# Kernel optimization log

Hardware: AMD Instinct MI355X
Metric: run time of the kernel (lower is better)

The kernel has to match this reference:

```python
import jax, jax.numpy as jnp
import numpy as np

E = 16        # num_experts
H = 1024      # hidden_size
I = 768       # moe_intermediate_size
TOP_K = 2     # num_experts_per_tok
B, S = 1, 2048


def setup_inputs() -> dict:
    key = jax.random.key(0)
    ks = jax.random.split(key, 5)
    scale = 0.02
    return {
        "hidden_states": jax.random.normal(ks[0], (B, S, H), dtype=jnp.float32),
        "gate_w": jax.random.normal(ks[1], (E, H), dtype=jnp.float32) * scale,
        "gate_proj": jax.random.normal(ks[2], (E, I, H), dtype=jnp.float32) * scale,
        "up_proj": jax.random.normal(ks[3], (E, I, H), dtype=jnp.float32) * scale,
        "down_proj": jax.random.normal(ks[4], (E, H, I), dtype=jnp.float32) * scale,
    }


def reference(hidden_states, gate_w, gate_proj, up_proj, down_proj):
    b, s, h = hidden_states.shape
    x = hidden_states.reshape(-1, h)                        # [T, H]
    T = x.shape[0]

    # Router: logits -> fp32 softmax -> top-k -> renormalize (norm_topk_prob=True)
    router_logits = x @ gate_w.T                            # [T, E]
    probs = jax.nn.softmax(router_logits.astype(jnp.float32), axis=-1)
    top_vals, top_idx = jax.lax.top_k(probs, TOP_K)         # [T, k]
    top_vals = top_vals / jnp.sum(top_vals, axis=-1, keepdims=True)

    # Dense combine-weight matrix [T, E] (zero for unrouted experts)
    rw = jnp.zeros((T, E), dtype=jnp.float32)
    rw = rw.at[jnp.arange(T)[:, None], top_idx].add(top_vals)
    rw = rw.astype(hidden_states.dtype)

    # Expert SwiGLU MLPs (dense-over-experts reference for the grouped GEMM)
    g = jnp.einsum("th,eih->eti", x, gate_proj)             # [E, T, I]
    u = jnp.einsum("th,eih->eti", x, up_proj)               # [E, T, I]
    hmid = jax.nn.silu(g) * u                                # [E, T, I]
    expert_out = jnp.einsum("eti,ehi->eth", hmid, down_proj)  # [E, T, H]

    # Weighted combine
    out = jnp.einsum("eth,te->th", expert_out, rw)          # [T, H]
    return out.reshape(b, s, h)
```

## Files before the change

kernel.cpp:

```cpp
#include <hip/hip_runtime.h>
#include <hip/hip_bf16.h>
#include <cmath>

constexpr int T = 2048;
constexpr int H = 1024;
constexpr int I = 768;
constexpr int E = 16;
constexpr int WMAX = 48;

constexpr int CVT_ITEMS = 768 * 3;
constexpr int RTR_BLOCKS = T / 8;
constexpr int CS = 2056;

typedef short short8  __attribute__((ext_vector_type(8)));
typedef short short4v __attribute__((ext_vector_type(4)));
typedef float f32x4   __attribute__((ext_vector_type(4)));

__device__ __forceinline__ short f2bf(float f) {
    __hip_bfloat16 h = __float2bfloat16(f);
    return *reinterpret_cast<short*>(&h);
}

__device__ __forceinline__ short8 pack8(float4 a, float4 b) {
    short8 v = {f2bf(a.x), f2bf(a.y), f2bf(a.z), f2bf(a.w),
                f2bf(b.x), f2bf(b.y), f2bf(b.z), f2bf(b.w)};
    return v;
}

__device__ __forceinline__ int sw(int r, int kg) {
    return r * 32 + (((kg + (r >> 1)) & 3) << 3);
}

__device__ __forceinline__ bool find_item(const int* __restrict__ cnt, int bx,
                                          int& e_o, int& t0_o, int& n_o) {
    int c = 0;
    #pragma unroll
    for (int e = 0; e < E; ++e) {
        int n = cnt[e];
        int m = (n + 127) >> 7;
        if (bx < c + m) { e_o = e; t0_o = (bx - c) << 7; n_o = n; return true; }
        c += m;
    }
    return false;
}

__global__ __launch_bounds__(256) void prep_kernel(
    const float* __restrict__ x,
    const float* __restrict__ gw,
    const float* __restrict__ gp,
    const float* __restrict__ up,
    const float* __restrict__ dp,
    short* __restrict__ xb,
    short* __restrict__ wtg,
    short* __restrict__ wtu,
    short* __restrict__ wtd,
    int* __restrict__ cnt,
    int* __restrict__ entries,
    float* __restrict__ wlist)
{
    __shared__ short lds[8 * CS];
    __shared__ float lg[8][16][2];

    const int tid = threadIdx.x;
    const int bid = blockIdx.x;

    if (bid < CVT_ITEMS) {
        const float* src; short* dst; int K;
        if (bid < 1536) {
            const int mat = bid >= 768;
            const int id3 = mat ? bid - 768 : bid;
            const int e = id3 / 48, rem = id3 - e * 48;
            const int rb = rem >> 2, kq = rem & 3;
            K = H;
            src = (mat ? up : gp) + (size_t)e * I * H + (size_t)(rb * 64) * H + kq * 256;
            dst = (mat ? wtu : wtg) + ((size_t)(e * 12 + rb) * 32 + kq * 8) * 2048;
        } else {
            const int id3 = bid - 1536;
            const int e = id3 / 48, rem = id3 - e * 48;
            const int rb = rem / 3, kq = rem - rb * 3;
            K = I;
            src = dp + (size_t)e * H * I + (size_t)(rb * 64) * I + kq * 256;
            dst = wtd + ((size_t)(e * 16 + rb) * 24 + kq * 8) * 2048;
        }

        #pragma unroll
        for (int it = 0; it < 16; ++it) {
            const int r  = it * 4 + (tid >> 6);
            const int kk = (tid & 63) * 4;
            float4 v = *(const float4*)(src + (size_t)r * K + kk);
            short4v s = {f2bf(v.x), f2bf(v.y), f2bf(v.z), f2bf(v.w)};
            *(short4v*)&lds[(kk >> 5) * CS + r * 32 + (kk & 31)] = s;
        }
        __syncthreads();
        #pragma unroll
        for (int j = 0; j < 8; ++j)
            *(short8*)(dst + j * 2048 + tid * 8) =
                *(const short8*)&lds[j * CS + tid * 8];
        return;
    }

    const int rb  = bid - CVT_ITEMS;
    const int tl = tid & 7;
    const int e  = (tid >> 3) & 15;
    const int hf = tid >> 7;
    const int t  = rb * 8 + tl;

    const float4* xr = (const float4*)(x + (size_t)t * H);
    const float4* gr = (const float4*)(gw + (size_t)e * H);
    short* xrow = xb + (size_t)t * H;

    float s0 = 0.f, s1 = 0.f;
    const int qlo = hf * 128, qhi = qlo + 128;
    #pragma unroll 8
    for (int q = qlo; q < qhi; q += 2) {
        float4 a = xr[q],     b = gr[q];
        float4 c = xr[q + 1], d = gr[q + 1];
        s0 += a.x * b.x + a.y * b.y + a.z * b.z + a.w * b.w;
        s1 += c.x * d.x + c.y * d.y + c.z * d.z + c.w * d.w;
        if (((q >> 3) & 15) == e)
            *(short8*)(xrow + q * 4) = pack8(a, c);
    }

    lg[tl][e][hf] = s0 + s1;
    __syncthreads();

    if (tid < 8) {
        int tk = rb * 8 + tid;
        float v1 = -3.0e38f, v2 = -3.0e38f;
        int i1 = 0, i2 = 0;
        #pragma unroll
        for (int k = 0; k < E; ++k) {
            float v = lg[tid][k][0] + lg[tid][k][1];
            if (v > v1) { v2 = v1; i2 = i1; v1 = v; i1 = k; }
            else if (v > v2) { v2 = v; i2 = k; }
        }
        float w1 = 1.f / (1.f + expf(v2 - v1));
        float w2 = 1.f - w1;
        int p = atomicAdd(&cnt[i1], 1);
        entries[i1 * T + p] = tk * 2;
        wlist[i1 * T + p] = w1;
        p = atomicAdd(&cnt[i2], 1);
        entries[i2 * T + p] = tk * 2 + 1;
        wlist[i2 * T + p] = w2;
    }
}

__global__ __launch_bounds__(256) void gateup_mfma(
    const short* __restrict__ xb,
    const short* __restrict__ wtg,
    const short* __restrict__ wtu,
    const int* __restrict__ cnt,
    const int* __restrict__ entries,
    short* __restrict__ hmid)
{
    int e, t0, n;
    if (!find_item(cnt, blockIdx.x, e, t0, n)) return;
    const int i0 = blockIdx.y * 64;

    __shared__ short Xs[128 * 32];
    __shared__ short Gs[64 * 32];
    __shared__ short Us[64 * 32];
    __shared__ int toks[128];

    const int tid = threadIdx.x;
    if (tid < 128) {
        int r = t0 + tid;
        toks[tid] = (r < n) ? entries[e * T + r] : -1;
    }
    __syncthreads();

    const int lane = tid & 63, wave = tid >> 6;
    const int m16 = lane & 15, q = lane >> 4;

    const int sr = tid >> 2, skg = tid & 3;
    const int xt0 = toks[sr], xt1 = toks[64 + sr];
    const short* xsrc0 = xb + (size_t)((xt0 >= 0 ? xt0 : 0) >> 1) * H + skg * 8;
    const short* xsrc1 = xb + (size_t)((xt1 >= 0 ? xt1 : 0) >> 1) * H + skg * 8;
    const short* gts = wtg + ((size_t)(e * 12 + blockIdx.y) * 32) * 2048 + tid * 8;
    const short* uts = wtu + ((size_t)(e * 12 + blockIdx.y) * 32) * 2048 + tid * 8;

    f32x4 accg[8], accu[8];
    #pragma unroll
    for (int a = 0; a < 8; ++a) {
        accg[a] = (f32x4){0.f, 0.f, 0.f, 0.f};
        accu[a] = (f32x4){0.f, 0.f, 0.f, 0.f};
    }

    short8 xc0 = *(const short8*)xsrc0;
    short8 xc1 = *(const short8*)xsrc1;
    short8 gt = *(const short8*)gts;
    short8 ut = *(const short8*)uts;

    for (int ks = 0; ks < H / 32; ++ks) {
        *(short8*)&Xs[sw(sr, skg)]      = xc0;
        *(short8*)&Xs[sw(64 + sr, skg)] = xc1;
        *(short8*)&Gs[sw(sr, skg)] = gt;
        *(short8*)&Us[sw(sr, skg)] = ut;
        int ksn = (ks + 1 < H / 32) ? ks + 1 : 0;
        int kn = ksn * 32;
        xc0 = *(const short8*)(xsrc0 + kn);
        xc1 = *(const short8*)(xsrc1 + kn);
        gt = *(const short8*)(gts + ksn * 2048);
        ut = *(const short8*)(uts + ksn * 2048);
        __syncthreads();

        short8 bg = *(const short8*)&Gs[sw(wave * 16 + m16, q)];
        short8 bu = *(const short8*)&Us[sw(wave * 16 + m16, q)];
        #pragma unroll
        for (int mi = 0; mi < 8; ++mi) {
            short8 af = *(const short8*)&Xs[sw(mi * 16 + m16, q)];
            accg[mi] = __builtin_amdgcn_mfma_f32_16x16x32_bf16(af, bg, accg[mi], 0, 0, 0);
            accu[mi] = __builtin_amdgcn_mfma_f32_16x16x32_bf16(af, bu, accu[mi], 0, 0, 0);
        }
        __syncthreads();
    }

    const int col = i0 + wave * 16 + m16;
    #pragma unroll
    for (int mi = 0; mi < 8; ++mi)
        #pragma unroll
        for (int j = 0; j < 4; ++j) {
            int row = mi * 16 + q * 4 + j;
            int slot = toks[row];
            if (slot < 0) continue;
            float g = accg[mi][j];
            float u = accu[mi][j];
            float hv = g / (1.f + expf(-g)) * u;
            ((unsigned short*)hmid)[(size_t)slot * I + col] = (unsigned short)f2bf(hv);
        }
}

__global__ __launch_bounds__(256) void down_mfma(
    const short* __restrict__ hmid,
    const short* __restrict__ wtd,
    const int* __restrict__ cnt,
    const int* __restrict__ entries,
    const float* __restrict__ wlist,
    float* __restrict__ out)
{
    int e, t0, n;
    if (!find_item(cnt, blockIdx.x, e, t0, n)) return;
    const int h0 = blockIdx.y * 64;

    __shared__ short As[128 * 32];
    __shared__ short Bs[64 * 32];
    __shared__ int toks[128];
    __shared__ float wr[128];

    const int tid = threadIdx.x;
    if (tid < 128) {
        int r = t0 + tid;
        bool v = (r < n);
        toks[tid] = v ? entries[e * T + r] : -1;
        wr[tid]   = v ? wlist[e * T + r] : 0.f;
    }
    __syncthreads();

    const int lane = tid & 63, wave = tid >> 6;
    const int m16 = lane & 15, q = lane >> 4;

    const int sr = tid >> 2, skg = tid & 3;
    const int at0 = toks[sr], at1 = toks[64 + sr];
    const short* asrc0 = hmid + (size_t)(at0 >= 0 ? at0 : 0) * I + skg * 8;
    const short* asrc1 = hmid + (size_t)(at1 >= 0 ? at1 : 0) * I + skg * 8;
    const short* bts = wtd + ((size_t)(e * 16 + blockIdx.y) * 24) * 2048 + tid * 8;

    f32x4 acc[8];
    #pragma unroll
    for (int a = 0; a < 8; ++a) acc[a] = (f32x4){0.f, 0.f, 0.f, 0.f};

    short8 ac0 = *(const short8*)asrc0;
    short8 ac1 = *(const short8*)asrc1;
    short8 bt = *(const short8*)bts;

    for (int ks = 0; ks < I / 32; ++ks) {
        *(short8*)&As[sw(sr, skg)]      = ac0;
        *(short8*)&As[sw(64 + sr, skg)] = ac1;
        *(short8*)&Bs[sw(sr, skg)]      = bt;
        int ksn = (ks + 1 < I / 32) ? ks + 1 : 0;
        int kn = ksn * 32;
        ac0 = *(const short8*)(asrc0 + kn);
        ac1 = *(const short8*)(asrc1 + kn);
        bt = *(const short8*)(bts + ksn * 2048);
        __syncthreads();

        short8 bf = *(const short8*)&Bs[sw(wave * 16 + m16, q)];
        #pragma unroll
        for (int mi = 0; mi < 8; ++mi) {
            short8 af = *(const short8*)&As[sw(mi * 16 + m16, q)];
            acc[mi] = __builtin_amdgcn_mfma_f32_16x16x32_bf16(af, bf, acc[mi], 0, 0, 0);
        }
        __syncthreads();
    }

    const int col = h0 + wave * 16 + m16;
    #pragma unroll
    for (int mi = 0; mi < 8; ++mi)
        #pragma unroll
        for (int j = 0; j < 4; ++j) {
            int row = mi * 16 + q * 4 + j;
            int slot = toks[row];
            if (slot < 0) continue;
            atomicAdd(&out[(size_t)(slot >> 1) * H + col], wr[row] * acc[mi][j]);
        }
}

extern "C" void kernel_launch(void* const* d_in, const int* in_sizes, int n_in,
                              void* d_out, int out_size, void* d_ws, size_t ws_size,
                              hipStream_t stream) {
    const float* x  = (const float*)d_in[0];
    const float* gw = (const float*)d_in[1];
    const float* gp = (const float*)d_in[2];
    const float* up = (const float*)d_in[3];
    const float* dp = (const float*)d_in[4];
    float* out = (float*)d_out;

    char* ws = (char*)d_ws;
    int*   cnt     = (int*)ws;
    int*   entries = (int*)(ws + 2048);
    float* wlist   = (float*)(ws + 2048 + 131072);
    short* xb      = (short*)(ws + 2048 + 262144);
    short* hmid    = xb + (size_t)T * H;
    short* wtg     = hmid + (size_t)2 * T * I;
    short* wtu     = wtg + (size_t)E * I * H;
    short* wtd     = wtu + (size_t)E * I * H;

    hipMemsetAsync(ws, 0, 2048, stream);
    hipMemsetAsync(out, 0, (size_t)T * H * sizeof(float), stream);

    prep_kernel<<<CVT_ITEMS + RTR_BLOCKS, 256, 0, stream>>>(
        x, gw, gp, up, dp, xb, wtg, wtu, wtd, cnt, entries, wlist);
    gateup_mfma<<<dim3(WMAX, I / 64), 256, 0, stream>>>(
        xb, wtg, wtu, cnt, entries, hmid);
    down_mfma<<<dim3(WMAX, H / 64), 256, 0, stream>>>(
        hmid, wtd, cnt, entries, wlist, out);
}
```

Baseline: 285.1 us.

## Overlap down-proj weight conversion with gate/up GEMM and drop LDS transpose staging

Moves the fp32-to-bf16 conversion of down_proj weights out of the prep kernel and into extra blocks of the gate/up GEMM launch, so that conversion runs concurrently with the grouped GEMM. The gate/up weight conversion becomes a grid-stride loop that writes each converted element straight to its swizzled tiled position, with no LDS staging or block barrier. The intent is to shorten the serial prep stage and fill idle compute units during the GEMM. In exchange, the direct stores are narrow scattered 8-byte writes, and the converter blocks compete with the GEMM blocks for bandwidth and CUs.

```diff
diff --git a/kernel.cpp b/kernel.cpp
--- a/kernel.cpp
+++ b/kernel.cpp
@@ -8,9 +8,9 @@
 constexpr int E = 16;
 constexpr int WMAX = 48;
 
-constexpr int CVT_ITEMS = 768 * 3;
+constexpr int GU_BLOCKS = 2048;
 constexpr int RTR_BLOCKS = T / 8;
-constexpr int CS = 2056;
+constexpr int DW_XTRA = 86;
 
 typedef short short8  __attribute__((ext_vector_type(8)));
 typedef short short4v __attribute__((ext_vector_type(4)));
@@ -44,62 +44,44 @@
     return false;
 }
 
-__global__ __launch_bounds__(256) void prep_kernel(
+__global__ __launch_bounds__(256) void prep_gu(
     const float* __restrict__ x,
     const float* __restrict__ gw,
     const float* __restrict__ gp,
     const float* __restrict__ up,
-    const float* __restrict__ dp,
     short* __restrict__ xb,
     short* __restrict__ wtg,
     short* __restrict__ wtu,
-    short* __restrict__ wtd,
     int* __restrict__ cnt,
     int* __restrict__ entries,
     float* __restrict__ wlist)
 {
-    __shared__ short lds[8 * CS];
     __shared__ float lg[8][16][2];
-
     const int tid = threadIdx.x;
     const int bid = blockIdx.x;
 
-    if (bid < CVT_ITEMS) {
-        const float* src; short* dst; int K;
-        if (bid < 1536) {
-            const int mat = bid >= 768;
-            const int id3 = mat ? bid - 768 : bid;
-            const int e = id3 / 48, rem = id3 - e * 48;
-            const int rb = rem >> 2, kq = rem & 3;
-            K = H;
-            src = (mat ? up : gp) + (size_t)e * I * H + (size_t)(rb * 64) * H + kq * 256;
-            dst = (mat ? wtu : wtg) + ((size_t)(e * 12 + rb) * 32 + kq * 8) * 2048;
-        } else {
-            const int id3 = bid - 1536;
-            const int e = id3 / 48, rem = id3 - e * 48;
-            const int rb = rem / 3, kq = rem - rb * 3;
-            K = I;
-            src = dp + (size_t)e * H * I + (size_t)(rb * 64) * I + kq * 256;
-            dst = wtd + ((size_t)(e * 16 + rb) * 24 + kq * 8) * 2048;
-        }
-
-        #pragma unroll
-        for (int it = 0; it < 16; ++it) {
-            const int r  = it * 4 + (tid >> 6);
-            const int kk = (tid & 63) * 4;
-            float4 v = *(const float4*)(src + (size_t)r * K + kk);
+    if (bid < GU_BLOCKS) {
+        const int N4 = (E * I * H) / 4;
+        const int stride = GU_BLOCKS * 256;
+        #pragma unroll 2
+        for (int l4 = bid * 256 + tid; l4 < 2 * N4; l4 += stride) {
+            const bool isu = (l4 >= N4);
+            const int l = (isu ? l4 - N4 : l4) << 2;
+            const float* src = isu ? up : gp;
+            short* dst = isu ? wtu : wtg;
+            float4 v = *(const float4*)(src + l);
+            int e = l / (I * H);
+            int rem = l - e * (I * H);
+            int i = rem >> 10, kk = rem & 1023;
+            int chunk = ((e * 12 + (i >> 6)) * 32 + (kk >> 5)) << 11;
+            int pos = chunk + (((i & 63) << 2) + ((kk >> 3) & 3)) * 8 + (kk & 7);
             short4v s = {f2bf(v.x), f2bf(v.y), f2bf(v.z), f2bf(v.w)};
-            *(short4v*)&lds[(kk >> 5) * CS + r * 32 + (kk & 31)] = s;
-        }
-        __syncthreads();
-        #pragma unroll
-        for (int j = 0; j < 8; ++j)
-            *(short8*)(dst + j * 2048 + tid * 8) =
-                *(const short8*)&lds[j * CS + tid * 8];
+            *(short4v*)(dst + pos) = s;
+        }
         return;
     }
 
-    const int rb  = bid - CVT_ITEMS;
+    const int rb = bid - GU_BLOCKS;
     const int tl = tid & 7;
     const int e  = (tid >> 3) & 15;
     const int hf = tid >> 7;
@@ -149,10 +131,33 @@
     const short* __restrict__ xb,
     const short* __restrict__ wtg,
     const short* __restrict__ wtu,
+    const float* __restrict__ dp,
+    short* __restrict__ wtd,
     const int* __restrict__ cnt,
     const int* __restrict__ entries,
     short* __restrict__ hmid)
 {
+    const int tid = threadIdx.x;
+
+    if (blockIdx.x >= WMAX) {
+        const int v = (blockIdx.x - WMAX) * 12 + blockIdx.y;
+        const int N4 = (E * H * I) / 4;
+        const int stride = DW_XTRA * 12 * 256;
+        #pragma unroll 2
+        for (int l4 = v * 256 + tid; l4 < N4; l4 += stride) {
+            const int l = l4 << 2;
+            float4 w = *(const float4*)(dp + l);
+            int e = l / (H * I);
+            int rem = l - e * (H * I);
+            int h = rem / 768, kk = rem - h * 768;
+            int chunk = ((e * 16 + (h >> 6)) * 24 + (kk >> 5)) << 11;
+            int pos = chunk + (((h & 63) << 2) + ((kk >> 3) & 3)) * 8 + (kk & 7);
+            short4v s = {f2bf(w.x), f2bf(w.y), f2bf(w.z), f2bf(w.w)};
+            *(short4v*)(wtd + pos) = s;
+        }
+        return;
+    }
+
     int e, t0, n;
     if (!find_item(cnt, blockIdx.x, e, t0, n)) return;
     const int i0 = blockIdx.y * 64;
@@ -162,7 +167,6 @@
     __shared__ short Us[64 * 32];
     __shared__ int toks[128];
 
-    const int tid = threadIdx.x;
     if (tid < 128) {
         int r = t0 + tid;
         toks[tid] = (r < n) ? entries[e * T + r] : -1;
@@ -328,10 +332,10 @@
     hipMemsetAsync(ws, 0, 2048, stream);
     hipMemsetAsync(out, 0, (size_t)T * H * sizeof(float), stream);
 
-    prep_kernel<<<CVT_ITEMS + RTR_BLOCKS, 256, 0, stream>>>(
-        x, gw, gp, up, dp, xb, wtg, wtu, wtd, cnt, entries, wlist);
-    gateup_mfma<<<dim3(WMAX, I / 64), 256, 0, stream>>>(
-        xb, wtg, wtu, cnt, entries, hmid);
+    prep_gu<<<GU_BLOCKS + RTR_BLOCKS, 256, 0, stream>>>(
+        x, gw, gp, up, xb, wtg, wtu, cnt, entries, wlist);
+    gateup_mfma<<<dim3(WMAX + DW_XTRA, 12), 256, 0, stream>>>(
+        xb, wtg, wtu, dp, wtd, cnt, entries, hmid);
     down_mfma<<<dim3(WMAX, H / 64), 256, 0, stream>>>(
         hmid, wtd, cnt, entries, wlist, out);
 }
```

New measurement: 297.8 us. +4.5%, slower.
